# Kernel optimization log

Hardware: AMD Instinct MI355X
Metric: run time of the kernel (lower is better)

## Reference

```python
import jax, jax.numpy as jnp
import numpy as np

N_NODES = 100000
N_EDGES = 1200000
D = 64

def _mlp(x, w1, b1, w2, b2):
    # Linear -> tanh -> Linear (hidden activation tanh, no output activation)
    h = jnp.tanh(x @ w1 + b1)
    return h @ w2 + b2

def setup_inputs() -> dict:
    key = jax.random.key(0)
    ks = jax.random.split(key, 12)
    s = 1.0 / np.sqrt(D)
    inp = {
        "idx_i": jax.random.randint(ks[0], (N_EDGES,), 0, N_NODES, dtype=jnp.int32),
        "idx_j": jax.random.randint(ks[1], (N_EDGES,), 0, N_NODES, dtype=jnp.int32),
        "p1": jax.random.normal(ks[2], (N_NODES, D), dtype=jnp.float32),
        "basis": jax.random.normal(ks[3], (N_EDGES, D), dtype=jnp.float32),
    }
    names = ["pp_w1", "pp_w2", "pi_w1", "pi_w2", "ii_w1", "ii_w2"]
    for i, nm in enumerate(names):
        inp[nm] = jax.random.normal(ks[4 + i], (D, D), dtype=jnp.float32) * s
    for nm in ["pp_b1", "pp_b2", "pi_b1", "pi_b2", "ii_b1", "ii_b2"]:
        inp[nm] = jnp.zeros((D,), dtype=jnp.float32)
    return inp

def reference(idx_i, idx_j, p1, basis,
              pp_w1, pp_b1, pp_w2, pp_b2,
              pi_w1, pi_b1, pi_w2, pi_b2,
              ii_w1, ii_b1, ii_w2, ii_b2):
    # pp: per-node MLP
    pp1 = _mlp(p1, pp_w1, pp_b1, pp_w2, pp_b2)            # [N, D]
    # pi: gather both endpoints, fuse with basis, per-edge MLP
    inter = pp1[idx_i] + basis + pp1[idx_j]               # [E, D]
    pi1 = _mlp(inter, pi_w1, pi_b1, pi_w2, pi_b2)         # [E, D]
    # ii: per-edge MLP
    ii1 = _mlp(pi1, ii_w1, ii_b1, ii_w2, ii_b2)           # [E, D]
    # ip: scatter-add edge messages back to nodes
    ip1 = jax.ops.segment_sum(ii1, idx_i, num_segments=N_NODES)  # [N, D]
    return ip1
```

## Files before the change

kernel.cpp:

```cpp
#include <hip/hip_runtime.h>
#include <hip/hip_bf16.h>

#define DD 64

using f32x4 = __attribute__((ext_vector_type(4))) float;
using bfrag = __attribute__((ext_vector_type(8))) short;
using u32x4 = __attribute__((ext_vector_type(4))) unsigned int;

__device__ __forceinline__ short f2bf(float f) {
    __hip_bfloat16 h = __float2bfloat16(f);
    return *reinterpret_cast<short*>(&h);
}
__device__ __forceinline__ float tanh_fast(float x) {
    float e = __expf(-2.f * x);
    return __fdividef(2.f, 1.f + e) - 1.f;
}
__device__ __forceinline__ unsigned int pack2(float a, float b) {
    unsigned int lo = (unsigned int)(unsigned short)f2bf(a);
    unsigned int hi = (unsigned int)(unsigned short)f2bf(b);
    return lo | (hi << 16);
}
template <int CTRL>
__device__ __forceinline__ int dpp_i(int x) {
    return __builtin_amdgcn_update_dpp(0, x, CTRL, 0xF, 0xF, true);
}
template <int CTRL>
__device__ __forceinline__ float dpp_f(float x) {
    return __int_as_float(__builtin_amdgcn_update_dpp(0, __float_as_int(x), CTRL, 0xF, 0xF, true));
}

__global__ void prep_weights(const float* __restrict__ w0, const float* __restrict__ w1,
                             const float* __restrict__ w2, const float* __restrict__ w3,
                             const float* __restrict__ w4, const float* __restrict__ w5,
                             unsigned short* __restrict__ wfrag)
{
    int t = blockIdx.x * blockDim.x + threadIdx.x;
    if (t >= 6 * 4096) return;
    int l = t >> 12, r = t & 4095;
    int j = r & 7, lane = (r >> 3) & 63, ks = (r >> 9) & 1, dt = r >> 10;
    int k = ks * 32 + (lane >> 4) * 8 + j;
    int d = dt * 16 + (lane & 15);
    const float* W[6] = {w0, w1, w2, w3, w4, w5};
    wfrag[t] = (unsigned short)f2bf(W[l][k * DD + d]);
}

__device__ __forceinline__ void mfma_layer(const unsigned short* __restrict__ s_w, int layer,
                                           int lane, const float* __restrict__ s_bias, int g,
                                           bfrag B0, bfrag B1, f32x4 acc[4])
{
#pragma unroll
    for (int dt = 0; dt < 4; ++dt) {
        f32x4 a = *(const f32x4*)&s_bias[dt * 16 + g * 4];
        bfrag A0 = *(const bfrag*)&s_w[(layer * 8 + dt * 2 + 0) * 512 + lane * 8];
        bfrag A1 = *(const bfrag*)&s_w[(layer * 8 + dt * 2 + 1) * 512 + lane * 8];
        a = __builtin_amdgcn_mfma_f32_16x16x32_bf16(A0, B0, a, 0, 0, 0);
        a = __builtin_amdgcn_mfma_f32_16x16x32_bf16(A1, B1, a, 0, 0, 0);
        acc[dt] = a;
    }
}

template <bool ACT>
__device__ __forceinline__ void h_roundtrip(char* H, int swz, int m, int g,
                                            f32x4 acc[4], bfrag B[2])
{
#pragma unroll
    for (int dt = 0; dt < 4; ++dt) {
        float t0, t1, t2, t3;
        if (ACT) {
            t0 = tanh_fast(acc[dt][0]); t1 = tanh_fast(acc[dt][1]);
            t2 = tanh_fast(acc[dt][2]); t3 = tanh_fast(acc[dt][3]);
        } else {
            t0 = acc[dt][0]; t1 = acc[dt][1]; t2 = acc[dt][2]; t3 = acc[dt][3];
        }
        uint2 w;
        w.x = pack2(t0, t1);
        w.y = pack2(t2, t3);
        *(uint2*)(H + ((m * 128 + dt * 32 + g * 8) ^ swz)) = w;
    }
#pragma unroll
    for (int ks = 0; ks < 2; ++ks)
        B[ks] = *(const bfrag*)(H + ((m * 128 + ks * 64 + g * 16) ^ swz));
}

__global__ __launch_bounds__(256) void node_mfma_kernel(
    const float* __restrict__ p1,
    const unsigned short* __restrict__ wfrag,
    const float* __restrict__ b1, const float* __restrict__ b2,
    unsigned short* __restrict__ pp1, int n_rows)
{
    __shared__ __align__(16) unsigned short s_w[2 * 4096];
    __shared__ __align__(16) float s_b[2][DD];
    __shared__ __align__(16) unsigned short s_h[4][1024];

    int tid = threadIdx.x;
    {
        const u32x4* src = (const u32x4*)wfrag;
        u32x4* dst = (u32x4*)s_w;
        for (int i = tid; i < 2 * 4096 / 8; i += 256) dst[i] = src[i];
    }
    if (tid < DD) { s_b[0][tid] = b1[tid]; s_b[1][tid] = b2[tid]; }
    __syncthreads();

    int wave = tid >> 6, lane = tid & 63;
    int g = lane >> 4, m = lane & 15;
    char* H = (char*)s_h[wave];
    int swz = (m & 7) << 4;

    int gw = blockIdx.x * 4 + wave;
    int nw = gridDim.x * 4;
    int ntiles = (n_rows + 15) >> 4;

    for (int t = gw; t < ntiles; t += nw) {
        int row = t * 16 + m;
        int rc = min(row, n_rows - 1);
        bfrag B[2];
#pragma unroll
        for (int ks = 0; ks < 2; ++ks) {
            int f0 = ks * 32 + g * 8;
            f32x4 x0 = *(const f32x4*)(p1 + (size_t)rc * DD + f0);
            f32x4 x1 = *(const f32x4*)(p1 + (size_t)rc * DD + f0 + 4);
#pragma unroll
            for (int j = 0; j < 4; ++j) { B[ks][j] = f2bf(x0[j]); B[ks][j + 4] = f2bf(x1[j]); }
        }
        f32x4 acc[4];
        mfma_layer(s_w, 0, lane, s_b[0], g, B[0], B[1], acc);
        h_roundtrip<true>(H, swz, m, g, acc, B);
        mfma_layer(s_w, 1, lane, s_b[1], g, B[0], B[1], acc);
        if (row < n_rows) {
#pragma unroll
            for (int dt = 0; dt < 4; ++dt) {
                unsigned int* dst = (unsigned int*)((char*)pp1 + (size_t)row * 128 + dt * 32 + g * 8);
                dst[0] = pack2(acc[dt][0], acc[dt][1]);
                dst[1] = pack2(acc[dt][2], acc[dt][3]);
            }
        }
    }
}

__global__ void hist_kernel(const int* __restrict__ idx_i, int* __restrict__ counts, int n) {
    int base = (blockIdx.x * 256 + threadIdx.x) * 4;
    if (base + 3 < n) {
        int4 v = *(const int4*)(idx_i + base);
        atomicAdd(&counts[v.x], 1); atomicAdd(&counts[v.y], 1);
        atomicAdd(&counts[v.z], 1); atomicAdd(&counts[v.w], 1);
    } else {
        for (int e = base; e < n; ++e) atomicAdd(&counts[idx_i[e]], 1);
    }
}

__global__ void chunk_reduce(const int* __restrict__ counts, int* __restrict__ csum, int n) {
    __shared__ int red[256];
    int b = blockIdx.x, t = threadIdx.x;
    int base = b * 1024 + t * 4, s = 0;
#pragma unroll
    for (int j = 0; j < 4; ++j) { int i = base + j; s += (i < n) ? counts[i] : 0; }
    red[t] = s; __syncthreads();
    for (int off = 128; off; off >>= 1) { if (t < off) red[t] += red[t + off]; __syncthreads(); }
    if (!t) csum[b] = red[0];
}

__global__ void scan_tops(const int* __restrict__ csum, int* __restrict__ cbase, int nchunks) {
    __shared__ int s[256];
    int t = threadIdx.x;
    int v = (t < nchunks) ? csum[t] : 0;
    s[t] = v; __syncthreads();
    for (int d = 1; d < 256; d <<= 1) {
        int x = s[t];
        if (t >= d) x += s[t - d];
        __syncthreads();
        s[t] = x;
        __syncthreads();
    }
    if (t < nchunks) cbase[t] = s[t] - v;
}

__global__ void chunk_scan(const int* __restrict__ counts, const int* __restrict__ cbase,
                           int* __restrict__ cursor, int n) {
    __shared__ int sums[256];
    int b = blockIdx.x, t = threadIdx.x;
    int base = b * 1024 + t * 4;
    int v[4], s = 0;
#pragma unroll
    for (int j = 0; j < 4; ++j) { v[j] = (base + j < n) ? counts[base + j] : 0; s += v[j]; }
    sums[t] = s; __syncthreads();
    for (int d = 1; d < 256; d <<= 1) {
        int x = sums[t];
        if (t >= d) x += sums[t - d];
        __syncthreads();
        sums[t] = x;
        __syncthreads();
    }
    int excl = sums[t] - s + cbase[b];
#pragma unroll
    for (int j = 0; j < 4; ++j) {
        if (base + j < n) cursor[base + j] = excl;
        excl += v[j];
    }
}

__global__ void bin_kernel(const int* __restrict__ idx_i, const int* __restrict__ idx_j,
                           int* __restrict__ cursor, int4* __restrict__ sorted, int n) {
    int base = (blockIdx.x * 256 + threadIdx.x) * 4;
    if (base + 3 < n) {
        int4 vi = *(const int4*)(idx_i + base);
        int4 vj = *(const int4*)(idx_j + base);
        int p;
        p = atomicAdd(&cursor[vi.x], 1); sorted[p] = make_int4(vi.x, vj.x, base + 0, 0);
        p = atomicAdd(&cursor[vi.y], 1); sorted[p] = make_int4(vi.y, vj.y, base + 1, 0);
        p = atomicAdd(&cursor[vi.z], 1); sorted[p] = make_int4(vi.z, vj.z, base + 2, 0);
        p = atomicAdd(&cursor[vi.w], 1); sorted[p] = make_int4(vi.w, vj.w, base + 3, 0);
    } else {
        for (int e = base; e < n; ++e) {
            int ni = idx_i[e];
            int p = atomicAdd(&cursor[ni], 1);
            sorted[p] = make_int4(ni, idx_j[e], e, 0);
        }
    }
}

struct Gath {
    u32x4 piA, piB, pjA, pjB;
    f32x4 b0, b1, b2, b3;
};

__device__ __forceinline__ int4 load_rec(const int4* __restrict__ sorted, int t, int m, int n_edges) {
    int gm = t * 16 + m;
    return sorted[min(gm, n_edges - 1)];
}

__device__ __forceinline__ Gath issue_gather(const int4& rec,
                                             const unsigned short* __restrict__ pp1,
                                             const float* __restrict__ basis, int g)
{
    Gath G;
    const unsigned* pi_p = (const unsigned*)(pp1 + (size_t)rec.x * DD);
    const unsigned* pj_p = (const unsigned*)(pp1 + (size_t)rec.y * DD);
    const float* bs = basis + (size_t)rec.z * DD;
    G.piA = *(const u32x4*)(pi_p + g * 4);
    G.piB = *(const u32x4*)(pi_p + 16 + g * 4);
    G.pjA = *(const u32x4*)(pj_p + g * 4);
    G.pjB = *(const u32x4*)(pj_p + 16 + g * 4);
    G.b0 = *(const f32x4*)(bs + g * 8);
    G.b1 = *(const f32x4*)(bs + g * 8 + 4);
    G.b2 = *(const f32x4*)(bs + 32 + g * 8);
    G.b3 = *(const f32x4*)(bs + 32 + g * 8 + 4);
    return G;
}

__device__ __forceinline__ void build_B(const Gath& G, bfrag B[2])
{
    float bf[16];
    *(f32x4*)&bf[0] = G.b0; *(f32x4*)&bf[4] = G.b1;
    *(f32x4*)&bf[8] = G.b2; *(f32x4*)&bf[12] = G.b3;
    u32x4 pi[2] = {G.piA, G.piB};
    u32x4 pj[2] = {G.pjA, G.pjB};
#pragma unroll
    for (int ks = 0; ks < 2; ++ks) {
#pragma unroll
        for (int w = 0; w < 4; ++w) {
            unsigned upi = pi[ks][w], upj = pj[ks][w];
            float lo = __uint_as_float(upi << 16) + bf[ks * 8 + 2 * w]
                     + __uint_as_float(upj << 16);
            float hi = __uint_as_float(upi & 0xFFFF0000u) + bf[ks * 8 + 2 * w + 1]
                     + __uint_as_float(upj & 0xFFFF0000u);
            B[ks][2 * w]     = f2bf(lo);
            B[ks][2 * w + 1] = f2bf(hi);
        }
    }
}

__global__ __launch_bounds__(256) void edge_sorted_kernel(
    const int4* __restrict__ sorted,
    const unsigned short* __restrict__ pp1,
    const float* __restrict__ basis,
    const unsigned short* __restrict__ wfrag,
    const float* __restrict__ pi_b1, const float* __restrict__ pi_b2,
    const float* __restrict__ ii_b1, const float* __restrict__ ii_b2,
    float* __restrict__ out, int n_edges, int ntiles)
{
    __shared__ __align__(16) unsigned short s_w[4 * 4096];
    __shared__ __align__(16) float s_b[4][DD];
    __shared__ __align__(16) unsigned short s_h[4][1024];

    int tid = threadIdx.x;
    {
        const u32x4* src = (const u32x4*)(wfrag + 2 * 4096);
        u32x4* dst = (u32x4*)s_w;
        for (int i = tid; i < 4 * 4096 / 8; i += 256) dst[i] = src[i];
    }
    if (tid < DD) {
        s_b[0][tid] = pi_b1[tid]; s_b[1][tid] = pi_b2[tid];
        s_b[2][tid] = ii_b1[tid]; s_b[3][tid] = ii_b2[tid];
    }
    __syncthreads();

    int wave = tid >> 6, lane = tid & 63;
    int g = lane >> 4, m = lane & 15;
    char* H = (char*)s_h[wave];
    int swz = (m & 7) << 4;

    int nwaves = gridDim.x * 4;
    int w = blockIdx.x * 4 + wave;
    int tpw = (ntiles + nwaves - 1) / nwaves;
    int t0 = w * tpw;
    int t1 = min(t0 + tpw, ntiles);
    if (t0 >= t1) return;

    int id_before = (t0 > 0) ? sorted[t0 * 16 - 1].x : -2;

    int cur = -9;
    float carry[16];
#pragma unroll
    for (int i = 0; i < 16; ++i) carry[i] = 0.f;

    int4 rec_c = load_rec(sorted, t0, m, n_edges);
    int4 rec_n = load_rec(sorted, t0 + 1, m, n_edges);
    Gath gc = issue_gather(rec_c, pp1, basis, g);

    for (int t = t0; t < t1; ++t) {
        int ne = (t + 1) * 16;
        int nf_raw = __shfl(rec_n.x, 0);
        int next_first = (ne < n_edges) ? nf_raw : -3;

        int gm = t * 16 + m;
        int idv = (gm < n_edges) ? rec_c.x : -1;

        bfrag B[2];
        build_B(gc, B);
        int4 rec_n2 = load_rec(sorted, t + 2, m, n_edges);
        if (t + 1 < t1) gc = issue_gather(rec_n, pp1, basis, g);

        f32x4 acc[4];
        mfma_layer(s_w, 0, lane, s_b[0], g, B[0], B[1], acc);
        h_roundtrip<true>(H, swz, m, g, acc, B);
        mfma_layer(s_w, 1, lane, s_b[1], g, B[0], B[1], acc);
        h_roundtrip<false>(H, swz, m, g, acc, B);
        mfma_layer(s_w, 2, lane, s_b[2], g, B[0], B[1], acc);
        h_roundtrip<true>(H, swz, m, g, acc, B);
        mfma_layer(s_w, 3, lane, s_b[3], g, B[0], B[1], acc);

        float v[16];
#pragma unroll
        for (int i = 0; i < 16; ++i) v[i] = acc[i >> 2][i & 3];

        {
            int idS; float cm;
            idS = dpp_i<0x111>(idv); cm = ((m >= 1) && (idS == idv)) ? 1.f : 0.f;
#pragma unroll
            for (int i = 0; i < 16; ++i) { float sh = dpp_f<0x111>(v[i]); v[i] = fmaf(sh, cm, v[i]); }
            idS = dpp_i<0x112>(idv); cm = ((m >= 2) && (idS == idv)) ? 1.f : 0.f;
#pragma unroll
            for (int i = 0; i < 16; ++i) { float sh = dpp_f<0x112>(v[i]); v[i] = fmaf(sh, cm, v[i]); }
            idS = dpp_i<0x114>(idv); cm = ((m >= 4) && (idS == idv)) ? 1.f : 0.f;
#pragma unroll
            for (int i = 0; i < 16; ++i) { float sh = dpp_f<0x114>(v[i]); v[i] = fmaf(sh, cm, v[i]); }
            idS = dpp_i<0x118>(idv); cm = ((m >= 8) && (idS == idv)) ? 1.f : 0.f;
#pragma unroll
            for (int i = 0; i < 16; ++i) { float sh = dpp_f<0x118>(v[i]); v[i] = fmaf(sh, cm, v[i]); }
        }

        int id_next = dpp_i<0x101>(idv);
        bool last = (m == 15);
        bool closes = last ? (idv != next_first) : (idv != id_next);

        if (closes && idv == cur) {
#pragma unroll
            for (int i = 0; i < 16; ++i) v[i] += carry[i];
        }
        if (closes && idv >= 0) {
            size_t ob = (size_t)idv * DD;
            if (idv > id_before) {
#pragma unroll
                for (int dt = 0; dt < 4; ++dt) {
                    f32x4 sv = {v[dt * 4 + 0], v[dt * 4 + 1], v[dt * 4 + 2], v[dt * 4 + 3]};
                    *(f32x4*)&out[ob + (size_t)(dt * 16 + g * 4)] = sv;
                }
            } else {
#pragma unroll
                for (int i = 0; i < 16; ++i)
                    atomicAdd(&out[ob + (size_t)((i >> 2) * 16 + g * 4 + (i & 3))], v[i]);
            }
        }

        int id15 = __shfl(idv, 15);
        bool cont = (id15 == next_first);
        bool cont_carry = (id15 == cur);
        if (cont) {
#pragma unroll
            for (int i = 0; i < 16; ++i) {
                float s15 = __shfl(v[i], lane | 15);
                carry[i] = s15 + (cont_carry ? carry[i] : 0.f);
            }
        }
        cur = cont ? id15 : -9;

        rec_c = rec_n; rec_n = rec_n2;
    }

    if (cur >= 0 && m == 0) {
#pragma unroll
        for (int i = 0; i < 16; ++i)
            atomicAdd(&out[(size_t)cur * DD + (size_t)((i >> 2) * 16 + g * 4 + (i & 3))], carry[i]);
    }
}

extern "C" void kernel_launch(void* const* d_in, const int* in_sizes, int n_in,
                              void* d_out, int out_size, void* d_ws, size_t ws_size,
                              hipStream_t stream) {
    const int*   idx_i = (const int*)d_in[0];
    const int*   idx_j = (const int*)d_in[1];
    const float* p1    = (const float*)d_in[2];
    const float* basis = (const float*)d_in[3];
    const float* pp_w1 = (const float*)d_in[4];
    const float* pp_w2 = (const float*)d_in[5];
    const float* pi_w1 = (const float*)d_in[6];
    const float* pi_w2 = (const float*)d_in[7];
    const float* ii_w1 = (const float*)d_in[8];
    const float* ii_w2 = (const float*)d_in[9];
    const float* pp_b1 = (const float*)d_in[10];
    const float* pp_b2 = (const float*)d_in[11];
    const float* pi_b1 = (const float*)d_in[12];
    const float* pi_b2 = (const float*)d_in[13];
    const float* ii_b1 = (const float*)d_in[14];
    const float* ii_b2 = (const float*)d_in[15];

    int n_edges = in_sizes[0];
    int n_nodes = in_sizes[2] / DD;
    int ntiles  = (n_edges + 15) / 16;

    size_t off = 0;
    auto take = [&](size_t b) { size_t o = off; off += (b + 255) & ~(size_t)255; return o; };
    size_t o_wfrag  = take(6 * 4096 * 2);
    size_t o_pp1    = take((size_t)n_nodes * DD * 2);
    size_t o_counts = take((size_t)n_nodes * 4);
    size_t o_csum   = take(1024 * 4);
    size_t o_cbase  = take(1024 * 4);
    size_t o_cursor = take((size_t)n_nodes * 4);
    size_t o_sorted = take((size_t)ntiles * 16 * 16);
    (void)off;

    char* ws = (char*)d_ws;
    unsigned short* wfrag  = (unsigned short*)(ws + o_wfrag);
    unsigned short* pp1    = (unsigned short*)(ws + o_pp1);
    int*            counts = (int*)(ws + o_counts);
    int*            csum   = (int*)(ws + o_csum);
    int*            cbase  = (int*)(ws + o_cbase);
    int*            cursor = (int*)(ws + o_cursor);
    int4*           sorted = (int4*)(ws + o_sorted);
    float* out = (float*)d_out;

    hipMemsetAsync(d_out, 0, (size_t)out_size * sizeof(float), stream);
    hipMemsetAsync(counts, 0, (size_t)n_nodes * 4, stream);

    prep_weights<<<96, 256, 0, stream>>>(pp_w1, pp_w2, pi_w1, pi_w2, ii_w1, ii_w2, wfrag);
    node_mfma_kernel<<<512, 256, 0, stream>>>(p1, wfrag, pp_b1, pp_b2, pp1, n_nodes);

    int eg4 = (n_edges / 4 + 255) / 256 + 1;
    int nch = (n_nodes + 1023) / 1024;
    hist_kernel<<<eg4, 256, 0, stream>>>(idx_i, counts, n_edges);
    chunk_reduce<<<nch, 256, 0, stream>>>(counts, csum, n_nodes);
    scan_tops<<<1, 256, 0, stream>>>(csum, cbase, nch);
    chunk_scan<<<nch, 256, 0, stream>>>(counts, cbase, cursor, n_nodes);
    bin_kernel<<<eg4, 256, 0, stream>>>(idx_i, idx_j, cursor, sorted, n_edges);

    edge_sorted_kernel<<<768, 256, 0, stream>>>(sorted, pp1, basis, wfrag,
                                                pi_b1, pi_b2, ii_b1, ii_b2,
                                                out, n_edges, ntiles);
}
```

Baseline: 381.4 us.

## Fuse preprocessing kernels into one cooperative kernel and use packed bf16 conversion

Replaces two memsets, weight prep, histogram, two-level scan and binning with a single cooperative kernel that uses grid-wide syncs between phases. The goal is to remove several small kernel launches and the gaps between them. It also swaps scalar bf16 conversions for the v_cvt_pk_bf16_f32 instruction to pack two values at once. The cost is grid.sync barriers, less parallel non-vectorized atomic loops, and a scan chunk size of 512, which gives about 196 chunks and must stay at or below 256.

```diff
diff --git a/kernel.cpp b/kernel.cpp
--- a/kernel.cpp
+++ b/kernel.cpp
@@ -1,7 +1,9 @@
 #include <hip/hip_runtime.h>
 #include <hip/hip_bf16.h>
+#include <hip/hip_cooperative_groups.h>
 
 #define DD 64
+#define CH 512
 
 using f32x4 = __attribute__((ext_vector_type(4))) float;
 using bfrag = __attribute__((ext_vector_type(8))) short;
@@ -11,15 +13,15 @@
     __hip_bfloat16 h = __float2bfloat16(f);
     return *reinterpret_cast<short*>(&h);
 }
+__device__ __forceinline__ unsigned cvtpk(float a, float b) {
+    unsigned r;
+    asm("v_cvt_pk_bf16_f32 %0, %1, %2" : "=v"(r) : "v"(a), "v"(b));
+    return r;
+}
 __device__ __forceinline__ float tanh_fast(float x) {
     float e = __expf(-2.f * x);
     return __fdividef(2.f, 1.f + e) - 1.f;
 }
-__device__ __forceinline__ unsigned int pack2(float a, float b) {
-    unsigned int lo = (unsigned int)(unsigned short)f2bf(a);
-    unsigned int hi = (unsigned int)(unsigned short)f2bf(b);
-    return lo | (hi << 16);
-}
 template <int CTRL>
 __device__ __forceinline__ int dpp_i(int x) {
     return __builtin_amdgcn_update_dpp(0, x, CTRL, 0xF, 0xF, true);
@@ -29,19 +31,91 @@
     return __int_as_float(__builtin_amdgcn_update_dpp(0, __float_as_int(x), CTRL, 0xF, 0xF, true));
 }
 
-__global__ void prep_weights(const float* __restrict__ w0, const float* __restrict__ w1,
-                             const float* __restrict__ w2, const float* __restrict__ w3,
-                             const float* __restrict__ w4, const float* __restrict__ w5,
-                             unsigned short* __restrict__ wfrag)
-{
-    int t = blockIdx.x * blockDim.x + threadIdx.x;
-    if (t >= 6 * 4096) return;
-    int l = t >> 12, r = t & 4095;
-    int j = r & 7, lane = (r >> 3) & 63, ks = (r >> 9) & 1, dt = r >> 10;
-    int k = ks * 32 + (lane >> 4) * 8 + j;
-    int d = dt * 16 + (lane & 15);
-    const float* W[6] = {w0, w1, w2, w3, w4, w5};
-    wfrag[t] = (unsigned short)f2bf(W[l][k * DD + d]);
+__global__ __launch_bounds__(256) void build_kernel(
+    const int* __restrict__ idx_i, const int* __restrict__ idx_j,
+    const float* __restrict__ w0, const float* __restrict__ w1,
+    const float* __restrict__ w2, const float* __restrict__ w3,
+    const float* __restrict__ w4, const float* __restrict__ w5,
+    unsigned short* __restrict__ wfrag,
+    int* __restrict__ counts, int* __restrict__ csum, int* __restrict__ cbase,
+    int* __restrict__ cursor, int4* __restrict__ sorted,
+    float* __restrict__ out, int n_edges, int n_nodes, int out_elems)
+{
+    cooperative_groups::grid_group grid = cooperative_groups::this_grid();
+    int t = threadIdx.x;
+    int gid = blockIdx.x * 256 + t;
+    int gsz = gridDim.x * 256;
+    __shared__ int s[256];
+
+    for (int i = gid; i < (out_elems >> 2); i += gsz)
+        ((float4*)out)[i] = make_float4(0.f, 0.f, 0.f, 0.f);
+    for (int i = gid; i < n_nodes; i += gsz) counts[i] = 0;
+    {
+        const float* W[6] = {w0, w1, w2, w3, w4, w5};
+        for (int i = gid; i < 6 * 4096; i += gsz) {
+            int l = i >> 12, r = i & 4095;
+            int j = r & 7, lane = (r >> 3) & 63, ks = (r >> 9) & 1, dt = r >> 10;
+            int k = ks * 32 + (lane >> 4) * 8 + j;
+            int d = dt * 16 + (lane & 15);
+            wfrag[i] = (unsigned short)f2bf(W[l][k * DD + d]);
+        }
+    }
+    __threadfence();
+    grid.sync();
+
+    for (int e = gid; e < n_edges; e += gsz) atomicAdd(&counts[idx_i[e]], 1);
+    __threadfence();
+    grid.sync();
+
+    int nch = (n_nodes + CH - 1) / CH;
+
+    for (int c = blockIdx.x; c < nch; c += gridDim.x) {
+        int base = c * CH + t * 2;
+        int v0 = (base < n_nodes) ? counts[base] : 0;
+        int v1 = (base + 1 < n_nodes) ? counts[base + 1] : 0;
+        s[t] = v0 + v1; __syncthreads();
+        for (int d = 128; d; d >>= 1) { if (t < d) s[t] += s[t + d]; __syncthreads(); }
+        if (!t) csum[c] = s[0];
+        __syncthreads();
+    }
+    __threadfence();
+    grid.sync();
+
+    if (blockIdx.x == 0) {
+        int v = (t < nch) ? csum[t] : 0;
+        s[t] = v; __syncthreads();
+        for (int d = 1; d < 256; d <<= 1) {
+            int x = s[t]; if (t >= d) x += s[t - d];
+            __syncthreads(); s[t] = x; __syncthreads();
+        }
+        if (t < nch) cbase[t] = s[t] - v;
+    }
+    __threadfence();
+    grid.sync();
+
+    for (int c = blockIdx.x; c < nch; c += gridDim.x) {
+        int base = c * CH + t * 2;
+        int v0 = (base < n_nodes) ? counts[base] : 0;
+        int v1 = (base + 1 < n_nodes) ? counts[base + 1] : 0;
+        int sv = v0 + v1;
+        s[t] = sv; __syncthreads();
+        for (int d = 1; d < 256; d <<= 1) {
+            int x = s[t]; if (t >= d) x += s[t - d];
+            __syncthreads(); s[t] = x; __syncthreads();
+        }
+        int excl = s[t] - sv + cbase[c];
+        if (base < n_nodes) cursor[base] = excl;
+        if (base + 1 < n_nodes) cursor[base + 1] = excl + v0;
+        __syncthreads();
+    }
+    __threadfence();
+    grid.sync();
+
+    for (int e = gid; e < n_edges; e += gsz) {
+        int ni = idx_i[e];
+        int pos = atomicAdd(&cursor[ni], 1);
+        sorted[pos] = make_int4(ni, idx_j[e], e, 0);
+    }
 }
 
 __device__ __forceinline__ void mfma_layer(const unsigned short* __restrict__ s_w, int layer,
@@ -73,8 +147,8 @@
             t0 = acc[dt][0]; t1 = acc[dt][1]; t2 = acc[dt][2]; t3 = acc[dt][3];
         }
         uint2 w;
-        w.x = pack2(t0, t1);
-        w.y = pack2(t2, t3);
+        w.x = cvtpk(t0, t1);
+        w.y = cvtpk(t2, t3);
         *(uint2*)(H + ((m * 128 + dt * 32 + g * 8) ^ swz)) = w;
     }
 #pragma unroll
@@ -119,8 +193,12 @@
             int f0 = ks * 32 + g * 8;
             f32x4 x0 = *(const f32x4*)(p1 + (size_t)rc * DD + f0);
             f32x4 x1 = *(const f32x4*)(p1 + (size_t)rc * DD + f0 + 4);
-#pragma unroll
-            for (int j = 0; j < 4; ++j) { B[ks][j] = f2bf(x0[j]); B[ks][j + 4] = f2bf(x1[j]); }
+            u32x4 r;
+            r[0] = cvtpk(x0[0], x0[1]);
+            r[1] = cvtpk(x0[2], x0[3]);
+            r[2] = cvtpk(x1[0], x1[1]);
+            r[3] = cvtpk(x1[2], x1[3]);
+            B[ks] = *reinterpret_cast<bfrag*>(&r);
         }
         f32x4 acc[4];
         mfma_layer(s_w, 0, lane, s_b[0], g, B[0], B[1], acc);
@@ -130,90 +208,9 @@
 #pragma unroll
             for (int dt = 0; dt < 4; ++dt) {
                 unsigned int* dst = (unsigned int*)((char*)pp1 + (size_t)row * 128 + dt * 32 + g * 8);
-                dst[0] = pack2(acc[dt][0], acc[dt][1]);
-                dst[1] = pack2(acc[dt][2], acc[dt][3]);
+                dst[0] = cvtpk(acc[dt][0], acc[dt][1]);
+                dst[1] = cvtpk(acc[dt][2], acc[dt][3]);
             }
-        }
-    }
-}
-
-__global__ void hist_kernel(const int* __restrict__ idx_i, int* __restrict__ counts, int n) {
-    int base = (blockIdx.x * 256 + threadIdx.x) * 4;
-    if (base + 3 < n) {
-        int4 v = *(const int4*)(idx_i + base);
-        atomicAdd(&counts[v.x], 1); atomicAdd(&counts[v.y], 1);
-        atomicAdd(&counts[v.z], 1); atomicAdd(&counts[v.w], 1);
-    } else {
-        for (int e = base; e < n; ++e) atomicAdd(&counts[idx_i[e]], 1);
-    }
-}
-
-__global__ void chunk_reduce(const int* __restrict__ counts, int* __restrict__ csum, int n) {
-    __shared__ int red[256];
-    int b = blockIdx.x, t = threadIdx.x;
-    int base = b * 1024 + t * 4, s = 0;
-#pragma unroll
-    for (int j = 0; j < 4; ++j) { int i = base + j; s += (i < n) ? counts[i] : 0; }
-    red[t] = s; __syncthreads();
-    for (int off = 128; off; off >>= 1) { if (t < off) red[t] += red[t + off]; __syncthreads(); }
-    if (!t) csum[b] = red[0];
-}
-
-__global__ void scan_tops(const int* __restrict__ csum, int* __restrict__ cbase, int nchunks) {
-    __shared__ int s[256];
-    int t = threadIdx.x;
-    int v = (t < nchunks) ? csum[t] : 0;
-    s[t] = v; __syncthreads();
-    for (int d = 1; d < 256; d <<= 1) {
-        int x = s[t];
-        if (t >= d) x += s[t - d];
-        __syncthreads();
-        s[t] = x;
-        __syncthreads();
-    }
-    if (t < nchunks) cbase[t] = s[t] - v;
-}
-
-__global__ void chunk_scan(const int* __restrict__ counts, const int* __restrict__ cbase,
-                           int* __restrict__ cursor, int n) {
-    __shared__ int sums[256];
-    int b = blockIdx.x, t = threadIdx.x;
-    int base = b * 1024 + t * 4;
-    int v[4], s = 0;
-#pragma unroll
-    for (int j = 0; j < 4; ++j) { v[j] = (base + j < n) ? counts[base + j] : 0; s += v[j]; }
-    sums[t] = s; __syncthreads();
-    for (int d = 1; d < 256; d <<= 1) {
-        int x = sums[t];
-        if (t >= d) x += sums[t - d];
-        __syncthreads();
-        sums[t] = x;
-        __syncthreads();
-    }
-    int excl = sums[t] - s + cbase[b];
-#pragma unroll
-    for (int j = 0; j < 4; ++j) {
-        if (base + j < n) cursor[base + j] = excl;
-        excl += v[j];
-    }
-}
-
-__global__ void bin_kernel(const int* __restrict__ idx_i, const int* __restrict__ idx_j,
-                           int* __restrict__ cursor, int4* __restrict__ sorted, int n) {
-    int base = (blockIdx.x * 256 + threadIdx.x) * 4;
-    if (base + 3 < n) {
-        int4 vi = *(const int4*)(idx_i + base);
-        int4 vj = *(const int4*)(idx_j + base);
-        int p;
-        p = atomicAdd(&cursor[vi.x], 1); sorted[p] = make_int4(vi.x, vj.x, base + 0, 0);
-        p = atomicAdd(&cursor[vi.y], 1); sorted[p] = make_int4(vi.y, vj.y, base + 1, 0);
-        p = atomicAdd(&cursor[vi.z], 1); sorted[p] = make_int4(vi.z, vj.z, base + 2, 0);
-        p = atomicAdd(&cursor[vi.w], 1); sorted[p] = make_int4(vi.w, vj.w, base + 3, 0);
-    } else {
-        for (int e = base; e < n; ++e) {
-            int ni = idx_i[e];
-            int p = atomicAdd(&cursor[ni], 1);
-            sorted[p] = make_int4(ni, idx_j[e], e, 0);
         }
     }
 }
@@ -256,6 +253,7 @@
     u32x4 pj[2] = {G.pjA, G.pjB};
 #pragma unroll
     for (int ks = 0; ks < 2; ++ks) {
+        u32x4 r;
 #pragma unroll
         for (int w = 0; w < 4; ++w) {
             unsigned upi = pi[ks][w], upj = pj[ks][w];
@@ -263,9 +261,9 @@
                      + __uint_as_float(upj << 16);
             float hi = __uint_as_float(upi & 0xFFFF0000u) + bf[ks * 8 + 2 * w + 1]
                      + __uint_as_float(upj & 0xFFFF0000u);
-            B[ks][2 * w]     = f2bf(lo);
-            B[ks][2 * w + 1] = f2bf(hi);
-        }
+            r[w] = cvtpk(lo, hi);
+        }
+        B[ks] = *reinterpret_cast<bfrag*>(&r);
     }
 }
 
@@ -427,6 +425,7 @@
     int n_edges = in_sizes[0];
     int n_nodes = in_sizes[2] / DD;
     int ntiles  = (n_edges + 15) / 16;
+    int out_elems = out_size;
 
     size_t off = 0;
     auto take = [&](size_t b) { size_t o = off; off += (b + 255) & ~(size_t)255; return o; };
@@ -449,19 +448,21 @@
     int4*           sorted = (int4*)(ws + o_sorted);
     float* out = (float*)d_out;
 
-    hipMemsetAsync(d_out, 0, (size_t)out_size * sizeof(float), stream);
-    hipMemsetAsync(counts, 0, (size_t)n_nodes * 4, stream);
-
-    prep_weights<<<96, 256, 0, stream>>>(pp_w1, pp_w2, pi_w1, pi_w2, ii_w1, ii_w2, wfrag);
+    {
+        void* params[] = {
+            (void*)&idx_i, (void*)&idx_j,
+            (void*)&pp_w1, (void*)&pp_w2, (void*)&pi_w1, (void*)&pi_w2,
+            (void*)&ii_w1, (void*)&ii_w2,
+            (void*)&wfrag,
+            (void*)&counts, (void*)&csum, (void*)&cbase,
+            (void*)&cursor, (void*)&sorted,
+            (void*)&out, (void*)&n_edges, (void*)&n_nodes, (void*)&out_elems
+        };
+        hipLaunchCooperativeKernel((const void*)build_kernel, dim3(512), dim3(256),
+                                   params, 0, stream);
+    }
+
     node_mfma_kernel<<<512, 256, 0, stream>>>(p1, wfrag, pp_b1, pp_b2, pp1, n_nodes);
-
-    int eg4 = (n_edges / 4 + 255) / 256 + 1;
-    int nch = (n_nodes + 1023) / 1024;
-    hist_kernel<<<eg4, 256, 0, stream>>>(idx_i, counts, n_edges);
-    chunk_reduce<<<nch, 256, 0, stream>>>(counts, csum, n_nodes);
-    scan_tops<<<1, 256, 0, stream>>>(csum, cbase, nch);
-    chunk_scan<<<nch, 256, 0, stream>>>(counts, cbase, cursor, n_nodes);
-    bin_kernel<<<eg4, 256, 0, stream>>>(idx_i, idx_j, cursor, sorted, n_edges);
 
     edge_sorted_kernel<<<768, 256, 0, stream>>>(sorted, pp1, basis, wfrag,
                                                 pi_b1, pi_b2, ii_b1, ii_b2,
```

Measured after the change: 801.1 us. 2.1x slower.
